# Kernel optimization log

Measured on AMD Instinct MI355X. Metric: run time of the kernel, lower is better.

## Reference

```python
import jax, jax.numpy as jnp
import numpy as np

D_MODEL = 2048
N_HEADS = 16
QK_ROPE = 64
QK_NOPE = 128
KV_LORA = 512
V_DIM = 128
QK_DIM = QK_ROPE + QK_NOPE
RMS_EPS = 1.1920928955078125e-07  # torch fp32 finfo.eps (nn.RMSNorm default eps=None)


def apply_rope(x, base=10000.0):
    # x: [B, S, H, D] ; torchtune-style interleaved-pair rotary
    B, S, H, D = x.shape
    freqs = 1.0 / (base ** (jnp.arange(0, D, 2, dtype=jnp.float32) / D))  # [D/2]
    t = jnp.arange(S, dtype=jnp.float32)[:, None] * freqs[None, :]        # [S, D/2]
    cos = jnp.cos(t)[None, :, None, :]
    sin = jnp.sin(t)[None, :, None, :]
    x1 = x[..., 0::2]
    x2 = x[..., 1::2]
    out = jnp.stack([x1 * cos - x2 * sin, x2 * cos + x1 * sin], axis=-1)
    return out.reshape(B, S, H, D).astype(x.dtype)


def setup_inputs() -> dict:
    key = jax.random.key(0)
    ks = jax.random.split(key, 6)
    s = lambda fan_in: 1.0 / np.sqrt(fan_in)
    x = jax.random.normal(ks[0], (2, 2048, D_MODEL), dtype=jnp.float32)
    Wq = jax.random.normal(ks[1], (D_MODEL, N_HEADS * QK_DIM), dtype=jnp.float32) * s(D_MODEL)
    Wkv_a = jax.random.normal(ks[2], (D_MODEL, KV_LORA + QK_ROPE), dtype=jnp.float32) * s(D_MODEL)
    kv_norm_w = jnp.ones((KV_LORA,), dtype=jnp.float32)
    Wkv_b = jax.random.normal(ks[3], (KV_LORA, N_HEADS * (QK_NOPE + V_DIM)), dtype=jnp.float32) * s(KV_LORA)
    Wo = jax.random.normal(ks[4], (N_HEADS * V_DIM, D_MODEL), dtype=jnp.float32) * s(N_HEADS * V_DIM)
    return {"x": x, "Wq": Wq, "Wkv_a": Wkv_a, "kv_norm_w": kv_norm_w, "Wkv_b": Wkv_b, "Wo": Wo}


def reference(x, Wq, Wkv_a, kv_norm_w, Wkv_b, Wo):
    B, S, _ = x.shape
    # queries: split nope/rope, rotary on rope slice only
    q = (x @ Wq).reshape(B, S, N_HEADS, QK_DIM)
    q_nope, q_rope = q[..., :QK_NOPE], q[..., QK_NOPE:]
    q = jnp.concatenate([q_nope, apply_rope(q_rope)], axis=-1)  # [B,S,H,QK_DIM]
    # compressed kv + decoupled rope key
    kv = x @ Wkv_a                                              # [B,S,KV_LORA+QK_ROPE]
    c_kv, k_rope = kv[..., :KV_LORA], kv[..., KV_LORA:]
    k_rope = apply_rope(k_rope.reshape(B, S, 1, QK_ROPE))       # [B,S,1,QK_ROPE]
    # RMSNorm on compressed latent, then decompress
    c_kv = c_kv * jax.lax.rsqrt(jnp.mean(c_kv * c_kv, axis=-1, keepdims=True) + RMS_EPS) * kv_norm_w
    kv = (c_kv @ Wkv_b).reshape(B, S, N_HEADS, QK_NOPE + V_DIM)
    k_nope, v = kv[..., :QK_NOPE], kv[..., QK_NOPE:]
    k = jnp.concatenate([k_nope, jnp.broadcast_to(k_rope, (B, S, N_HEADS, QK_ROPE))], axis=-1)
    # causal SDPA over sequence dim
    scale = 1.0 / np.sqrt(QK_DIM)
    scores = jnp.einsum('bqhd,bkhd->bhqk', q, k) * scale        # [B,H,S,S]
    mask = jnp.tril(jnp.ones((S, S), dtype=bool))
    scores = jnp.where(mask, scores, jnp.finfo(scores.dtype).min)
    attn = jax.nn.softmax(scores, axis=-1)
    out = jnp.einsum('bhqk,bkhd->bqhd', attn, v).reshape(B, S, N_HEADS * V_DIM)
    return out @ Wo
```

## Files before the change

kernel.cpp:

```cpp
#include <hip/hip_runtime.h>
#include <hip/hip_bf16.h>
#include <math.h>

#define BATCH   2
#define SEQ     2048
#define DM      2048
#define NH      16
#define QKR     64
#define QKN     128
#define KVL     512
#define VD      128
#define QKD     192
#define KVA_LD  640
#define RMS_EPS 1.1920928955078125e-07f

typedef __bf16 bf16x8 __attribute__((ext_vector_type(8)));
typedef float  f32x4  __attribute__((ext_vector_type(4)));

__device__ __forceinline__ void async16(const __bf16* g, __bf16* l)
{
    __builtin_amdgcn_global_load_lds(
        (__attribute__((address_space(1))) unsigned int*)g,
        (__attribute__((address_space(3))) unsigned int*)l,
        16, 0, 0);
}

__global__ __launch_bounds__(256) void f32_to_bf16(const float* __restrict__ src,
                                                   __bf16* __restrict__ dst)
{
    int i = (blockIdx.x * 256 + threadIdx.x) * 4;
    float4 v = *reinterpret_cast<const float4*>(src + i);
    dst[i + 0] = (__bf16)v.x;
    dst[i + 1] = (__bf16)v.y;
    dst[i + 2] = (__bf16)v.z;
    dst[i + 3] = (__bf16)v.w;
}

__global__ __launch_bounds__(256) void transpose_w(const float* __restrict__ W,
                                                   __bf16* __restrict__ Wt,
                                                   int K, int N)
{
    __shared__ float t[64][65];
    const int n0 = blockIdx.x * 64, k0 = blockIdx.y * 64;
    const int tid = threadIdx.x;
    #pragma unroll
    for (int i = 0; i < 16; ++i) {
        int flat = i * 256 + tid;
        int kl = flat >> 6, nl = flat & 63;
        t[kl][nl] = (n0 + nl < N) ? W[(size_t)(k0 + kl) * N + n0 + nl] : 0.f;
    }
    __syncthreads();
    #pragma unroll
    for (int i = 0; i < 16; ++i) {
        int flat = i * 256 + tid;
        int nl = flat >> 6, kl = flat & 63;
        Wt[(size_t)(n0 + nl) * K + k0 + kl] = (__bf16)t[kl][nl];
    }
}

template<typename OT>
__global__ __launch_bounds__(256) void gemm_bf16(const __bf16* __restrict__ A,
                                                 const __bf16* __restrict__ Bt,
                                                 OT* __restrict__ C,
                                                 int K, int lda, int ldb, int ldc)
{
    __shared__ __bf16 As[128 * 32];
    __shared__ __bf16 Bs[128 * 32];
    const int tid = threadIdx.x;
    const int lane = tid & 63, wave = tid >> 6;
    const int n = lane & 15, quad = lane >> 4;
    const int row0 = blockIdx.y * 128, col0 = blockIdx.x * 128;
    const int wm = (wave >> 1) * 64, wn = (wave & 1) * 64;

    f32x4 acc[4][4];
    #pragma unroll
    for (int mi = 0; mi < 4; ++mi)
        #pragma unroll
        for (int ni = 0; ni < 4; ++ni)
            #pragma unroll
            for (int r = 0; r < 4; ++r) acc[mi][ni][r] = 0.f;

    const __bf16* Ag0 = A  + (size_t)(row0 + (tid >> 2)) * lda + (tid & 3) * 8;
    const __bf16* Bg0 = Bt + (size_t)(col0 + (tid >> 2)) * ldb + (tid & 3) * 8;
    const __bf16* Ag1 = Ag0 + (size_t)64 * lda;
    const __bf16* Bg1 = Bg0 + (size_t)64 * ldb;
    __bf16* As0 = As + tid * 8;        __bf16* As1 = As + (tid + 256) * 8;
    __bf16* Bs0 = Bs + tid * 8;        __bf16* Bs1 = Bs + (tid + 256) * 8;

    for (int k0 = 0; k0 < K; k0 += 32) {
        __syncthreads();
        async16(Ag0 + k0, As0);
        async16(Ag1 + k0, As1);
        async16(Bg0 + k0, Bs0);
        async16(Bg1 + k0, Bs1);
        __syncthreads();

        bf16x8 af[4], bfr[4];
        #pragma unroll
        for (int mi = 0; mi < 4; ++mi)
            af[mi] = *reinterpret_cast<const bf16x8*>(&As[(wm + mi * 16 + n) * 32 + quad * 8]);
        #pragma unroll
        for (int ni = 0; ni < 4; ++ni)
            bfr[ni] = *reinterpret_cast<const bf16x8*>(&Bs[(wn + ni * 16 + n) * 32 + quad * 8]);
        #pragma unroll
        for (int mi = 0; mi < 4; ++mi)
            #pragma unroll
            for (int ni = 0; ni < 4; ++ni)
                acc[mi][ni] = __builtin_amdgcn_mfma_f32_16x16x32_bf16(af[mi], bfr[ni], acc[mi][ni], 0, 0, 0);
    }

    #pragma unroll
    for (int mi = 0; mi < 4; ++mi)
        #pragma unroll
        for (int r = 0; r < 4; ++r) {
            OT* cp = C + (size_t)(row0 + wm + mi * 16 + quad * 4 + r) * ldc + col0 + wn + n;
            #pragma unroll
            for (int ni = 0; ni < 4; ++ni)
                cp[ni * 16] = (OT)acc[mi][ni][r];
        }
}

__global__ __launch_bounds__(256) void rope_q_kernel(__bf16* __restrict__ q)
{
    int idx = blockIdx.x * 256 + threadIdx.x;
    int i = idx & 31;
    int h = (idx >> 5) & 15;
    int s = (idx >> 9) & 2047;
    int b = idx >> 20;
    float t = (float)s * __expf(-(float)(2 * i) / 64.0f * 9.210340371976184f);
    float c = __cosf(t), sn = __sinf(t);
    __bf16* p = q + ((size_t)(b * SEQ + s)) * (NH * QKD) + h * QKD + QKN + 2 * i;
    float x1 = (float)p[0], x2 = (float)p[1];
    p[0] = (__bf16)(x1 * c - x2 * sn);
    p[1] = (__bf16)(x2 * c + x1 * sn);
}

__global__ __launch_bounds__(256) void rope_k_kernel(const float* __restrict__ kva,
                                                     __bf16* __restrict__ krope)
{
    int idx = blockIdx.x * 256 + threadIdx.x;
    int i = idx & 31;
    int s = (idx >> 5) & 2047;
    int b = idx >> 16;
    float t = (float)s * __expf(-(float)(2 * i) / 64.0f * 9.210340371976184f);
    float c = __cosf(t), sn = __sinf(t);
    const float* p = kva + ((size_t)(b * SEQ + s)) * KVA_LD + KVL + 2 * i;
    float x1 = p[0], x2 = p[1];
    __bf16* o = krope + ((size_t)(b * SEQ + s)) * QKR + 2 * i;
    o[0] = (__bf16)(x1 * c - x2 * sn);
    o[1] = (__bf16)(x2 * c + x1 * sn);
}

__global__ __launch_bounds__(256) void rmsnorm_kernel(const float* __restrict__ kva,
                                                      const float* __restrict__ w,
                                                      __bf16* __restrict__ out)
{
    const int rid = blockIdx.x;
    const float* row = kva + (size_t)rid * KVA_LD;
    const int tid = threadIdx.x;
    float v[2];
    float ss = 0.f;
    #pragma unroll
    for (int j = 0; j < 2; ++j) {
        int d = tid + j * 256;
        v[j] = row[d];
        ss += v[j] * v[j];
    }
    #pragma unroll
    for (int off = 32; off > 0; off >>= 1) ss += __shfl_down(ss, off, 64);
    __shared__ float red[4];
    if ((tid & 63) == 0) red[tid >> 6] = ss;
    __syncthreads();
    float total = red[0] + red[1] + red[2] + red[3];
    float scale = 1.0f / sqrtf(total * (1.0f / KVL) + RMS_EPS);
    #pragma unroll
    for (int j = 0; j < 2; ++j) {
        int d = tid + j * 256;
        out[(size_t)rid * KVL + d] = (__bf16)(v[j] * scale * w[d]);
    }
}

__global__ __launch_bounds__(256) void build_vt(const __bf16* __restrict__ kvb,
                                                __bf16* __restrict__ Vt)
{
    __shared__ __bf16 tile[64][136];
    const int s0 = blockIdx.x * 64, h = blockIdx.y, b = blockIdx.z;
    const int t = threadIdx.x;
    #pragma unroll
    for (int i = 0; i < 4; ++i) {
        int flat = i * 256 + t;
        int sl = flat >> 4, c8 = flat & 15;
        bf16x8 v = *reinterpret_cast<const bf16x8*>(
            &kvb[((size_t)(b * SEQ + s0 + sl)) * (NH * 256) + h * 256 + 128 + c8 * 8]);
        *reinterpret_cast<bf16x8*>(&tile[sl][c8 * 8]) = v;
    }
    __syncthreads();
    #pragma unroll
    for (int j = 0; j < 32; ++j) {
        int flat = j * 256 + t;
        int d = flat >> 6, sl = flat & 63;
        Vt[((size_t)((b * NH + h) * VD + d)) * SEQ + s0 + sl] = tile[sl][d];
    }
}

#define LKS 216
#define LVS 72
#define LPS 72
__global__ __launch_bounds__(256, 2) void attn_mfma(const __bf16* __restrict__ qb,
                                                    const __bf16* __restrict__ kvb,
                                                    const __bf16* __restrict__ krope,
                                                    const __bf16* __restrict__ Vt,
                                                    __bf16* __restrict__ ob)
{
    __shared__ __bf16 Ks[64 * LKS];
    __shared__ __bf16 Vs[128 * LVS];
    __shared__ __bf16 Ps[2][4 * 16 * LPS];
    const int tid = threadIdx.x;
    const int wave = tid >> 6, lane = tid & 63;
    const int n = lane & 15, quad = lane >> 4;
    const int pair = blockIdx.x, h = blockIdx.y, b = blockIdx.z;
    const int bh = b * NH + h;
    const float scale = 0.07216878364870323f;
    int qs[2];
    qs[0] = pair; qs[1] = 31 - pair;
    const int ntmax = qs[1] + 1;

    bf16x8 qfrag[2][6];
    #pragma unroll
    for (int s = 0; s < 2; ++s) {
        const int qrow = qs[s] * 64 + wave * 16 + n;
        const __bf16* qp = qb + ((size_t)(b * SEQ + qrow)) * (NH * QKD) + h * QKD + quad * 8;
        #pragma unroll
        for (int c = 0; c < 6; ++c)
            qfrag[s][c] = *reinterpret_cast<const bf16x8*>(qp + c * 32);
    }

    f32x4 Oa[2][8];
    float m_i[2][4], l_i[2][4];
    #pragma unroll
    for (int s = 0; s < 2; ++s) {
        #pragma unroll
        for (int i = 0; i < 8; ++i)
            #pragma unroll
            for (int r = 0; r < 4; ++r) Oa[s][i][r] = 0.f;
        #pragma unroll
        for (int r = 0; r < 4; ++r) { m_i[s][r] = -1e30f; l_i[s][r] = 0.f; }
    }

    int kkey[6], kc8[6];
    #pragma unroll
    for (int i = 0; i < 6; ++i) {
        int flat = i * 256 + tid;
        kkey[i] = flat / 24; kc8[i] = flat % 24;
    }
    const int vd = tid >> 3, vc8 = tid & 7;

    const __bf16* Vg = Vt + (size_t)bh * VD * SEQ;

    bf16x8 kpre[6], vpre[4];
    {
        const int k0 = 0;
        #pragma unroll
        for (int i = 0; i < 6; ++i) {
            const __bf16* src = (kc8[i] < 16)
                ? kvb + ((size_t)(b * SEQ + k0 + kkey[i])) * (NH * 256) + h * 256 + kc8[i] * 8
                : krope + ((size_t)(b * SEQ + k0 + kkey[i])) * QKR + (kc8[i] - 16) * 8;
            kpre[i] = *reinterpret_cast<const bf16x8*>(src);
        }
        #pragma unroll
        for (int i = 0; i < 4; ++i)
            vpre[i] = *reinterpret_cast<const bf16x8*>(Vg + (size_t)(vd + i * 32) * SEQ + k0 + vc8 * 8);
    }

    for (int kt = 0; kt < ntmax; ++kt) {
        __syncthreads();
        #pragma unroll
        for (int i = 0; i < 6; ++i)
            *reinterpret_cast<bf16x8*>(&Ks[kkey[i] * LKS + kc8[i] * 8]) = kpre[i];
        #pragma unroll
        for (int i = 0; i < 4; ++i)
            *reinterpret_cast<bf16x8*>(&Vs[(vd + i * 32) * LVS + vc8 * 8]) = vpre[i];
        __syncthreads();

        if (kt + 1 < ntmax) {
            const int k0n = (kt + 1) * 64;
            #pragma unroll
            for (int i = 0; i < 6; ++i) {
                const __bf16* src = (kc8[i] < 16)
                    ? kvb + ((size_t)(b * SEQ + k0n + kkey[i])) * (NH * 256) + h * 256 + kc8[i] * 8
                    : krope + ((size_t)(b * SEQ + k0n + kkey[i])) * QKR + (kc8[i] - 16) * 8;
                kpre[i] = *reinterpret_cast<const bf16x8*>(src);
            }
            #pragma unroll
            for (int i = 0; i < 4; ++i)
                vpre[i] = *reinterpret_cast<const bf16x8*>(Vg + (size_t)(vd + i * 32) * SEQ + k0n + vc8 * 8);
        }

        const int k0 = kt * 64;
        #pragma unroll
        for (int s = 0; s < 2; ++s) {
            if (kt > qs[s]) continue;

            f32x4 sacc[4];
            #pragma unroll
            for (int t = 0; t < 4; ++t) {
                f32x4 a;
                #pragma unroll
                for (int r = 0; r < 4; ++r) a[r] = 0.f;
                #pragma unroll
                for (int c = 0; c < 6; ++c) {
                    bf16x8 kf = *reinterpret_cast<const bf16x8*>(&Ks[(t * 16 + n) * LKS + c * 32 + quad * 8]);
                    a = __builtin_amdgcn_mfma_f32_16x16x32_bf16(qfrag[s][c], kf, a, 0, 0, 0);
                }
                sacc[t] = a;
            }

            const int qg = qs[s] * 64 + wave * 16 + quad * 4;
            const bool diag = (kt == qs[s]);
            float mloc[4];
            #pragma unroll
            for (int r = 0; r < 4; ++r) mloc[r] = -1e30f;
            #pragma unroll
            for (int t = 0; t < 4; ++t) {
                int key = k0 + t * 16 + n;
                #pragma unroll
                for (int r = 0; r < 4; ++r) {
                    float sv = sacc[t][r] * scale;
                    if (diag) sv = (key <= qg + r) ? sv : -1e30f;
                    sacc[t][r] = sv;
                    mloc[r] = fmaxf(mloc[r], sv);
                }
            }
            #pragma unroll
            for (int off = 1; off < 16; off <<= 1)
                #pragma unroll
                for (int r = 0; r < 4; ++r)
                    mloc[r] = fmaxf(mloc[r], __shfl_xor(mloc[r], off, 64));
            float alpha[4], sum[4];
            #pragma unroll
            for (int r = 0; r < 4; ++r) {
                float mn = fmaxf(m_i[s][r], mloc[r]);
                alpha[r] = __expf(m_i[s][r] - mn);
                m_i[s][r] = mn;
                sum[r] = 0.f;
            }
            #pragma unroll
            for (int t = 0; t < 4; ++t)
                #pragma unroll
                for (int r = 0; r < 4; ++r) {
                    float p = __expf(sacc[t][r] - m_i[s][r]);
                    sum[r] += p;
                    Ps[s][wave * 16 * LPS + (quad * 4 + r) * LPS + t * 16 + n] = (__bf16)p;
                }
            #pragma unroll
            for (int off = 1; off < 16; off <<= 1)
                #pragma unroll
                for (int r = 0; r < 4; ++r)
                    sum[r] += __shfl_xor(sum[r], off, 64);
            #pragma unroll
            for (int r = 0; r < 4; ++r) l_i[s][r] = l_i[s][r] * alpha[r] + sum[r];
            #pragma unroll
            for (int i = 0; i < 8; ++i)
                #pragma unroll
                for (int r = 0; r < 4; ++r) Oa[s][i][r] *= alpha[r];

            __asm__ volatile("s_waitcnt lgkmcnt(0)" ::: "memory");

            #pragma unroll
            for (int kc = 0; kc < 2; ++kc) {
                bf16x8 pf = *reinterpret_cast<const bf16x8*>(&Ps[s][wave * 16 * LPS + n * LPS + kc * 32 + quad * 8]);
                #pragma unroll
                for (int vt = 0; vt < 8; ++vt) {
                    bf16x8 vf = *reinterpret_cast<const bf16x8*>(&Vs[(vt * 16 + n) * LVS + kc * 32 + quad * 8]);
                    Oa[s][vt] = __builtin_amdgcn_mfma_f32_16x16x32_bf16(pf, vf, Oa[s][vt], 0, 0, 0);
                }
            }
        }
    }

    #pragma unroll
    for (int s = 0; s < 2; ++s)
        #pragma unroll
        for (int r = 0; r < 4; ++r) {
            float inv = 1.0f / l_i[s][r];
            int row = qs[s] * 64 + wave * 16 + quad * 4 + r;
            __bf16* op = ob + ((size_t)(b * SEQ + row)) * (NH * VD) + h * VD;
            #pragma unroll
            for (int vt = 0; vt < 8; ++vt)
                op[vt * 16 + n] = (__bf16)(Oa[s][vt][r] * inv);
        }
}

extern "C" void kernel_launch(void* const* d_in, const int* in_sizes, int n_in,
                              void* d_out, int out_size, void* d_ws, size_t ws_size,
                              hipStream_t stream)
{
    const float* x         = (const float*)d_in[0];
    const float* Wq        = (const float*)d_in[1];
    const float* Wkv_a     = (const float*)d_in[2];
    const float* kv_norm_w = (const float*)d_in[3];
    const float* Wkv_b     = (const float*)d_in[4];
    const float* Wo        = (const float*)d_in[5];
    float* out = (float*)d_out;

    float* ws = (float*)d_ws;
    __bf16* q_bf   = (__bf16*)ws;
    float*  kv_a   = ws + 6291456;
    __bf16* kv_b   = (__bf16*)(ws + 8912896);
    float*  r3     = ws + 17301504;
    __bf16* xb     = (__bf16*)r3;
    __bf16* Vt     = (__bf16*)r3;
    float*  r4     = ws + 21495808;
    __bf16* Wq_t   = (__bf16*)r4;
    __bf16* Wkva_t = (__bf16*)(r4 + 3145728);
    __bf16* Wkvb_t = (__bf16*)(r4 + 3801088);
    __bf16* attn_o = (__bf16*)r4;
    __bf16* Wo_t   = (__bf16*)(ws + 27787264);
    __bf16* c_kv_n = (__bf16*)(ws + 29884416);
    __bf16* krope  = (__bf16*)(ws + 30932992);

    const int M = BATCH * SEQ;
    dim3 blk(256);

    f32_to_bf16<<<(M * DM) / 1024, blk, 0, stream>>>(x, xb);
    transpose_w<<<dim3(3072 / 64, 2048 / 64), blk, 0, stream>>>(Wq, Wq_t, DM, NH * QKD);
    transpose_w<<<dim3(640 / 64, 2048 / 64), blk, 0, stream>>>(Wkv_a, Wkva_t, DM, KVL + QKR);
    transpose_w<<<dim3(4096 / 64, 512 / 64), blk, 0, stream>>>(Wkv_b, Wkvb_t, KVL, NH * 256);
    transpose_w<<<dim3(2048 / 64, 2048 / 64), blk, 0, stream>>>(Wo, Wo_t, NH * VD, DM);

    gemm_bf16<__bf16><<<dim3(3072 / 128, M / 128), blk, 0, stream>>>(xb, Wq_t, q_bf, DM, DM, DM, NH * QKD);
    gemm_bf16<float><<<dim3(640 / 128, M / 128), blk, 0, stream>>>(xb, Wkva_t, kv_a, DM, DM, DM, KVA_LD);

    rope_q_kernel<<<(BATCH * SEQ * NH * 32) / 256, blk, 0, stream>>>(q_bf);
    rope_k_kernel<<<(BATCH * SEQ * 32) / 256, blk, 0, stream>>>(kv_a, krope);
    rmsnorm_kernel<<<M, blk, 0, stream>>>(kv_a, kv_norm_w, c_kv_n);

    gemm_bf16<__bf16><<<dim3(4096 / 128, M / 128), blk, 0, stream>>>(c_kv_n, Wkvb_t, kv_b, KVL, KVL, KVL, NH * 256);

    build_vt<<<dim3(SEQ / 64, NH, BATCH), blk, 0, stream>>>(kv_b, Vt);

    attn_mfma<<<dim3(16, NH, BATCH), blk, 0, stream>>>(q_bf, kv_b, krope, Vt, attn_o);

    gemm_bf16<float><<<dim3(2048 / 128, M / 128), blk, 0, stream>>>(attn_o, Wo_t, out, NH * VD, NH * VD, NH * VD, DM);
}
```

Baseline: 535.9 us.

## Split attention KV loop across two blocks and merge partials in combine kernel

Each attention block now handles only every other key tile (even or odd), doubling the grid from 512 to 1024 blocks. Each half writes unnormalized bf16 partial outputs plus per-row max and sum, and a new combine kernel merges them with log-sum-exp weights. The change also remaps block indices so heads are grouped per XCD, shrinks the K LDS stride and the P buffer, and raises launch bounds to 3 blocks per SM. In exchange it adds an extra kernel launch, partial-output traffic to global memory, and some extra rounding from storing unnormalized partials in bf16.

Result: slower. 718.4 us (+34.1%).

```diff
diff --git a/kernel.cpp b/kernel.cpp
--- a/kernel.cpp
+++ b/kernel.cpp
@@ -15,6 +15,7 @@
 #define RMS_EPS 1.1920928955078125e-07f
 
 typedef __bf16 bf16x8 __attribute__((ext_vector_type(8)));
+typedef __bf16 bf16x4 __attribute__((ext_vector_type(4)));
 typedef float  f32x4  __attribute__((ext_vector_type(4)));
 
 __device__ __forceinline__ void async16(const __bf16* g, __bf16* l)
@@ -203,27 +204,35 @@
     }
 }
 
-#define LKS 216
+#define LKS 200
 #define LVS 72
 #define LPS 72
-__global__ __launch_bounds__(256, 2) void attn_mfma(const __bf16* __restrict__ qb,
+#define OPHALF 8388608
+__global__ __launch_bounds__(256, 3) void attn_mfma(const __bf16* __restrict__ qb,
                                                     const __bf16* __restrict__ kvb,
                                                     const __bf16* __restrict__ krope,
                                                     const __bf16* __restrict__ Vt,
-                                                    __bf16* __restrict__ ob)
+                                                    __bf16* __restrict__ Op,
+                                                    float* __restrict__ Ml)
 {
     __shared__ __bf16 Ks[64 * LKS];
     __shared__ __bf16 Vs[128 * LVS];
-    __shared__ __bf16 Ps[2][4 * 16 * LPS];
+    __shared__ __bf16 Ps[4 * 16 * LPS];
     const int tid = threadIdx.x;
     const int wave = tid >> 6, lane = tid & 63;
     const int n = lane & 15, quad = lane >> 4;
-    const int pair = blockIdx.x, h = blockIdx.y, b = blockIdx.z;
+
+    const int j = blockIdx.x + 32 * (blockIdx.y + 16 * blockIdx.z);
+    const int xcd = j & 7, loc = j >> 3;
+    const int hb = xcd * 4 + (loc & 3);
+    const int slot = loc >> 2;
+    const int pair = slot >> 1, hf = slot & 1;
+    const int h = hb & 15, b = hb >> 4;
     const int bh = b * NH + h;
     const float scale = 0.07216878364870323f;
     int qs[2];
     qs[0] = pair; qs[1] = 31 - pair;
-    const int ntmax = qs[1] + 1;
+    const int ntmax = 32 - pair;
 
     bf16x8 qfrag[2][6];
     #pragma unroll
@@ -259,7 +268,7 @@
 
     bf16x8 kpre[6], vpre[4];
     {
-        const int k0 = 0;
+        const int k0 = hf * 64;
         #pragma unroll
         for (int i = 0; i < 6; ++i) {
             const __bf16* src = (kc8[i] < 16)
@@ -272,7 +281,7 @@
             vpre[i] = *reinterpret_cast<const bf16x8*>(Vg + (size_t)(vd + i * 32) * SEQ + k0 + vc8 * 8);
     }
 
-    for (int kt = 0; kt < ntmax; ++kt) {
+    for (int kt = hf; kt < ntmax; kt += 2) {
         __syncthreads();
         #pragma unroll
         for (int i = 0; i < 6; ++i)
@@ -282,8 +291,8 @@
             *reinterpret_cast<bf16x8*>(&Vs[(vd + i * 32) * LVS + vc8 * 8]) = vpre[i];
         __syncthreads();
 
-        if (kt + 1 < ntmax) {
-            const int k0n = (kt + 1) * 64;
+        if (kt + 2 < ntmax) {
+            const int k0n = (kt + 2) * 64;
             #pragma unroll
             for (int i = 0; i < 6; ++i) {
                 const __bf16* src = (kc8[i] < 16)
@@ -350,7 +359,7 @@
                 for (int r = 0; r < 4; ++r) {
                     float p = __expf(sacc[t][r] - m_i[s][r]);
                     sum[r] += p;
-                    Ps[s][wave * 16 * LPS + (quad * 4 + r) * LPS + t * 16 + n] = (__bf16)p;
+                    Ps[wave * 16 * LPS + (quad * 4 + r) * LPS + t * 16 + n] = (__bf16)p;
                 }
             #pragma unroll
             for (int off = 1; off < 16; off <<= 1)
@@ -368,7 +377,7 @@
 
             #pragma unroll
             for (int kc = 0; kc < 2; ++kc) {
-                bf16x8 pf = *reinterpret_cast<const bf16x8*>(&Ps[s][wave * 16 * LPS + n * LPS + kc * 32 + quad * 8]);
+                bf16x8 pf = *reinterpret_cast<const bf16x8*>(&Ps[wave * 16 * LPS + n * LPS + kc * 32 + quad * 8]);
                 #pragma unroll
                 for (int vt = 0; vt < 8; ++vt) {
                     bf16x8 vf = *reinterpret_cast<const bf16x8*>(&Vs[(vt * 16 + n) * LVS + kc * 32 + quad * 8]);
@@ -382,13 +391,41 @@
     for (int s = 0; s < 2; ++s)
         #pragma unroll
         for (int r = 0; r < 4; ++r) {
-            float inv = 1.0f / l_i[s][r];
             int row = qs[s] * 64 + wave * 16 + quad * 4 + r;
-            __bf16* op = ob + ((size_t)(b * SEQ + row)) * (NH * VD) + h * VD;
+            __bf16* op = Op + (size_t)hf * OPHALF + ((size_t)(b * SEQ + row) * NH + h) * VD;
             #pragma unroll
             for (int vt = 0; vt < 8; ++vt)
-                op[vt * 16 + n] = (__bf16)(Oa[s][vt][r] * inv);
+                op[vt * 16 + n] = (__bf16)Oa[s][vt][r];
+            if (n == 0) {
+                float* ml = Ml + (((size_t)hf * 4096 + b * SEQ + row) * NH + h) * 2;
+                ml[0] = m_i[s][r];
+                ml[1] = l_i[s][r];
+            }
         }
+}
+
+__global__ __launch_bounds__(256) void attn_combine(const __bf16* __restrict__ Op,
+                                                    const float* __restrict__ Ml,
+                                                    __bf16* __restrict__ ob)
+{
+    int idx = blockIdx.x * 256 + threadIdx.x;
+    int c4 = idx & 31;
+    int h  = (idx >> 5) & 15;
+    int row = idx >> 9;
+    const float* ml0 = Ml + ((size_t)row * NH + h) * 2;
+    const float* ml1 = Ml + (((size_t)4096 + row) * NH + h) * 2;
+    float m0 = ml0[0], l0 = ml0[1], m1 = ml1[0], l1 = ml1[1];
+    float m = fmaxf(m0, m1);
+    float w0 = __expf(m0 - m), w1 = __expf(m1 - m);
+    float inv = 1.0f / (w0 * l0 + w1 * l1);
+    size_t off = ((size_t)row * NH + h) * VD + c4 * 4;
+    bf16x4 o0 = *reinterpret_cast<const bf16x4*>(Op + off);
+    bf16x4 o1 = *reinterpret_cast<const bf16x4*>(Op + OPHALF + off);
+    bf16x4 o;
+    #pragma unroll
+    for (int i = 0; i < 4; ++i)
+        o[i] = (__bf16)((w0 * (float)o0[i] + w1 * (float)o1[i]) * inv);
+    *reinterpret_cast<bf16x4*>(ob + off) = o;
 }
 
 extern "C" void kernel_launch(void* const* d_in, const int* in_sizes, int n_in,
@@ -407,17 +444,18 @@
     __bf16* q_bf   = (__bf16*)ws;
     float*  kv_a   = ws + 6291456;
     __bf16* kv_b   = (__bf16*)(ws + 8912896);
-    float*  r3     = ws + 17301504;
-    __bf16* xb     = (__bf16*)r3;
-    __bf16* Vt     = (__bf16*)r3;
+    __bf16* xb     = (__bf16*)(ws + 17301504);
+    __bf16* Vt     = (__bf16*)(ws + 17301504);
     float*  r4     = ws + 21495808;
     __bf16* Wq_t   = (__bf16*)r4;
-    __bf16* Wkva_t = (__bf16*)(r4 + 3145728);
-    __bf16* Wkvb_t = (__bf16*)(r4 + 3801088);
+    __bf16* Wkva_t = (__bf16*)(ws + 24641536);
+    __bf16* Wkvb_t = (__bf16*)(ws + 25296896);
     __bf16* attn_o = (__bf16*)r4;
-    __bf16* Wo_t   = (__bf16*)(ws + 27787264);
-    __bf16* c_kv_n = (__bf16*)(ws + 29884416);
-    __bf16* krope  = (__bf16*)(ws + 30932992);
+    __bf16* Wo_t   = (__bf16*)(ws + 26345472);
+    __bf16* c_kv_n = (__bf16*)(ws + 28442624);
+    __bf16* krope  = (__bf16*)(ws + 29491200);
+    float*  Ml     = ws + 29622272;
+    __bf16* Op     = (__bf16*)(ws + 29884416);
 
     const int M = BATCH * SEQ;
     dim3 blk(256);
@@ -439,7 +477,8 @@
 
     build_vt<<<dim3(SEQ / 64, NH, BATCH), blk, 0, stream>>>(kv_b, Vt);
 
-    attn_mfma<<<dim3(16, NH, BATCH), blk, 0, stream>>>(q_bf, kv_b, krope, Vt, attn_o);
+    attn_mfma<<<dim3(32, NH, BATCH), blk, 0, stream>>>(q_bf, kv_b, krope, Vt, Op, Ml);
+    attn_combine<<<(M * NH * 32) / 256, blk, 0, stream>>>(Op, Ml, attn_o);
 
     gemm_bf16<float><<<dim3(2048 / 128, M / 128), blk, 0, stream>>>(attn_o, Wo_t, out, NH * VD, NH * VD, NH * VD, DM);
 }
```
